# Kernel optimization log

Measured on AMD Instinct MI355X. Metric: run time of the kernel, lower is better.

The kernel has to match this reference:

```python
import jax, jax.numpy as jnp
import numpy as np
import math

B, S, H = 2, 2048, 1024
NH, DK, DV = 16, 64, 64
PAD = 0
VOCAB = 32000


def setup_inputs() -> dict:
    key = jax.random.key(0)
    ks = jax.random.split(key, 6)
    batch = jax.random.normal(ks[0], (B, S, H), dtype=jnp.float32)
    input_ids = jax.random.randint(ks[1], (B, S), 1, VOCAB)
    n_pad = S // 20
    input_ids = input_ids.at[:, S - n_pad:].set(PAD)
    init = 1.0 / math.sqrt(H)  # xavier-ish scale
    W_Q = jax.random.normal(ks[2], (H, NH * DK), dtype=jnp.float32) * init
    W_K = jax.random.normal(ks[3], (H, NH * DK), dtype=jnp.float32) * init
    W_V = jax.random.normal(ks[4], (H, NH * DV), dtype=jnp.float32) * init
    W_O = jax.random.normal(ks[5], (NH * DV, H), dtype=jnp.float32) * init
    return {
        "batch": batch, "input_ids": input_ids,
        "W_Q": W_Q, "W_K": W_K, "W_V": W_V,
        "b_Q": jnp.zeros((NH * DK,), jnp.float32),
        "b_K": jnp.zeros((NH * DK,), jnp.float32),
        "b_V": jnp.zeros((NH * DV,), jnp.float32),
        "W_O": W_O, "b_O": jnp.zeros((H,), jnp.float32),
    }


def reference(batch, input_ids, W_Q, W_K, W_V, b_Q, b_K, b_V, W_O, b_O):
    Bn, Sn, _ = batch.shape
    NEG = jnp.float32(-jnp.inf)
    # causal mask [S,S]: 0 where i>=j else -inf
    i = jnp.arange(Sn)
    causal = jnp.where(i[:, None] >= i[None, :], 0.0, NEG).astype(batch.dtype)
    # padding mask [B,1,S]: -inf at pad key positions
    pad = jnp.where(input_ids == PAD, NEG, 0.0).astype(batch.dtype)
    mask = causal[None, :, :] + pad[:, None, :]  # [B,S,S]

    Q = (batch @ W_Q + b_Q).reshape(Bn, Sn, NH, DK)
    K = (batch @ W_K + b_K).reshape(Bn, Sn, NH, DK)
    V = (batch @ W_V + b_V).reshape(Bn, Sn, NH, DV)

    scores = jnp.einsum('bqhd,bkhd->bhqk', Q, K) / math.sqrt(DK)
    attn = jax.nn.softmax(scores + mask[:, None, :, :], axis=-1)
    out = jnp.einsum('bhqk,bkhd->bqhd', attn, V).reshape(Bn, Sn, NH * DV)
    return out @ W_O + b_O
```

## Files before the change

### kernel.cpp

```cpp
#include <hip/hip_runtime.h>
#include <stdint.h>


typedef unsigned short u16;
typedef __attribute__((ext_vector_type(8))) __bf16 bf16x8;
typedef __attribute__((ext_vector_type(4))) float f32x4;
typedef __attribute__((ext_vector_type(4))) short s16x4;
typedef __attribute__((ext_vector_type(8))) short s16x8;
typedef __attribute__((ext_vector_type(2))) uint32_t u32x2;

#define SCL 0.18033688011112042f

__device__ __forceinline__ u16 f2bf(float f) {
  union { float f; uint32_t u; } v; v.f = f;
  uint32_t r = v.u + 0x7FFFu + ((v.u >> 16) & 1u);
  return (u16)(r >> 16);
}

__device__ __forceinline__ void gl_lds16(const u16* g, u16* l) {
  auto gp = reinterpret_cast<const __attribute__((address_space(1))) uint32_t*>(
      reinterpret_cast<uintptr_t>(g));
  auto lp = reinterpret_cast<__attribute__((address_space(3))) uint32_t*>(
      reinterpret_cast<uintptr_t>(l));
  __builtin_amdgcn_global_load_lds(gp, lp, 16, 0, 0);
}

__global__ void k_prologue(const float* __restrict__ batch, const int* __restrict__ ids,
                           const float* __restrict__ W_Q, const float* __restrict__ W_K,
                           const float* __restrict__ W_V, const float* __restrict__ W_O,
                           u16* __restrict__ Xbf, u16* __restrict__ dqkv, u16* __restrict__ dwo,
                           unsigned long long* __restrict__ pb) {
  __shared__ float tile[32][33];
  const int bx = blockIdx.x, t = threadIdx.x;
  if (bx < 4096) {
    int idx = (bx * 256 + t) * 4;
    const float4 v = *reinterpret_cast<const float4*>(batch + idx);
    uint2 o;
    o.x = (uint32_t)f2bf(v.x) | ((uint32_t)f2bf(v.y) << 16);
    o.y = (uint32_t)f2bf(v.z) | ((uint32_t)f2bf(v.w) << 16);
    *reinterpret_cast<uint2*>(Xbf + idx) = o;
  } else if (bx < 8192) {
    int b2 = bx - 4096;
    int z = b2 >> 10;
    b2 &= 1023;
    const float* src = z == 0 ? W_Q : (z == 1 ? W_K : (z == 2 ? W_V : W_O));
    u16* dst = z < 3 ? dqkv + (size_t)z * 1024 * 1024 : dwo;
    int c0 = (b2 & 31) * 32, r0 = (b2 >> 5) * 32;
    int tx = t & 31, ty = t >> 5;
#pragma unroll
    for (int i = 0; i < 4; ++i)
      tile[ty + i * 8][tx] = src[(size_t)(r0 + ty + i * 8) * 1024 + c0 + tx];
    __syncthreads();
#pragma unroll
    for (int i = 0; i < 4; ++i)
      dst[(size_t)(c0 + ty + i * 8) * 1024 + r0 + tx] = f2bf(tile[tx][ty + i * 8]);
  } else {
    int idx = (bx - 8192) * 4 + (t >> 6);
    int ln = t & 63;
    int b = idx >> 5, j = idx & 31;
    unsigned long long m = __ballot(ids[b * 2048 + j * 64 + ln] == 0);
    if (ln == 0) pb[idx] = m;
  }
}


__device__ __forceinline__ void gemm_tile_acc(
    const u16* __restrict__ A, const u16* __restrict__ Bt, int K,
    int tm, int tn, u16* AsA, u16* BsA, f32x4 acc[4][4]) {
  const int t = threadIdx.x, wv = t >> 6, ln = t & 63;
  const int wr = (wv & 1) * 64, wc = (wv >> 1) * 64;
  const int lr = ln & 15, q8 = (ln >> 4) * 8;
  const int srow = ln >> 2, scol = (ln & 3) * 8;

  const u16* a0 = A  + (size_t)(tm + wv * 16 + srow) * K + scol;
  const u16* a1 = A  + (size_t)(tm + (wv + 4) * 16 + srow) * K + scol;
  const u16* b0 = Bt + (size_t)(tn + wv * 16 + srow) * K + scol;
  const u16* b1 = Bt + (size_t)(tn + (wv + 4) * 16 + srow) * K + scol;
  const int l0 = wv * 512 + ln * 8, l1 = (wv + 4) * 512 + ln * 8;

#define STAGE64(k0, ho)                                   \
  {                                                       \
    gl_lds16(a0 + (k0),      AsA + (ho) + l0);            \
    gl_lds16(a1 + (k0),      AsA + (ho) + l1);            \
    gl_lds16(a0 + (k0) + 32, AsA + (ho) + 4096 + l0);     \
    gl_lds16(a1 + (k0) + 32, AsA + (ho) + 4096 + l1);     \
    gl_lds16(b0 + (k0),      BsA + (ho) + l0);            \
    gl_lds16(b1 + (k0),      BsA + (ho) + l1);            \
    gl_lds16(b0 + (k0) + 32, BsA + (ho) + 4096 + l0);     \
    gl_lds16(b1 + (k0) + 32, BsA + (ho) + 4096 + l1);     \
  }

  STAGE64(0, 0);
  __syncthreads();

  int co = 0;
  for (int k0 = 0; k0 < K; k0 += 64) {
    if (k0 + 64 < K) STAGE64(k0 + 64, co ^ 8192);
#pragma unroll
    for (int s = 0; s < 2; ++s) {
      const u16* Asb = AsA + co + s * 4096;
      const u16* Bsb = BsA + co + s * 4096;
      bf16x8 av[4], bv[4];
#pragma unroll
      for (int m = 0; m < 4; ++m)
        av[m] = *reinterpret_cast<const bf16x8*>(Asb + (wr + m * 16 + lr) * 32 + q8);
#pragma unroll
      for (int n = 0; n < 4; ++n)
        bv[n] = *reinterpret_cast<const bf16x8*>(Bsb + (wc + n * 16 + lr) * 32 + q8);
#pragma unroll
      for (int m = 0; m < 4; ++m)
#pragma unroll
        for (int n = 0; n < 4; ++n)
          acc[m][n] = __builtin_amdgcn_mfma_f32_16x16x32_bf16(av[m], bv[n], acc[m][n], 0, 0, 0);
    }
    if (k0 + 64 < K) __syncthreads();
    co ^= 8192;
  }
#undef STAGE64
}

__global__ __launch_bounds__(256) void k_qkv(
    const u16* __restrict__ X, const u16* __restrict__ Wt,
    const float* __restrict__ bQ, const float* __restrict__ bK, const float* __restrict__ bV,
    u16* __restrict__ Qt, u16* __restrict__ Kt, u16* __restrict__ Vt) {
  __shared__ __align__(16) u16 AsA[2 * 8192];
  __shared__ __align__(16) u16 BsA[2 * 8192];
  f32x4 acc[4][4] = {};
  const int tm = blockIdx.x * 128, tn = blockIdx.y * 128;
  gemm_tile_acc(X, Wt, 1024, tm, tn, AsA, BsA, acc);

  const int t = threadIdx.x, wv = t >> 6, ln = t & 63;
  const int wr = (wv & 1) * 64, wc = (wv >> 1) * 64;
  const int lr = ln & 15, q4 = (ln >> 4) * 4;
  const int which = tn >> 10;

  if (which == 0) {
#pragma unroll
    for (int n = 0; n < 4; ++n) {
      int f = (tn + wc + n * 16 + lr) & 1023;
      float bb = bQ[f];
      int h = f >> 6, dd = f & 63;
      int kh = dd >> 5, qq = (dd & 31) >> 3, e = dd & 7;
#pragma unroll
      for (int m = 0; m < 4; ++m)
#pragma unroll
        for (int r = 0; r < 4; ++r) {
          int gr = tm + wr + m * 16 + q4 + r;
          int b = gr >> 11, s = gr & 2047;
          int bh = b * 16 + h;
          size_t addr = (((size_t)(bh * 64 + (s >> 5)) * 4 + ((s & 31) >> 4) * 2 + kh) << 9) +
                        ((s & 15) + 16 * qq) * 8 + e;
          Qt[addr] = f2bf((acc[m][n][r] + bb) * SCL);
        }
    }
  } else if (which == 1) {
#pragma unroll
    for (int n = 0; n < 4; ++n) {
      int f = (tn + wc + n * 16 + lr) & 1023;
      float bb = bK[f];
      int h = f >> 6, dd = f & 63;
      int kh = dd >> 5, qq = (dd & 31) >> 3, e = dd & 7;
#pragma unroll
      for (int m = 0; m < 4; ++m)
#pragma unroll
        for (int r = 0; r < 4; ++r) {
          int gr = tm + wr + m * 16 + q4 + r;
          int b = gr >> 11, s = gr & 2047;
          int bh = b * 16 + h;
          size_t addr = (((size_t)(bh * 32 + (s >> 6)) * 8 + kh * 4 + ((s & 63) >> 4)) << 9) +
                        ((s & 15) + 16 * qq) * 8 + e;
          Kt[addr] = f2bf(acc[m][n][r] + bb);
        }
    }
  } else {
#pragma unroll
    for (int n = 0; n < 4; ++n) {
      int f = (tn + wc + n * 16 + lr) & 1023;
      float bb = bV[f];
      int h = f >> 6, dd = f & 63;
      int md = dd >> 4, iv = dd & 15;
#pragma unroll
      for (int m = 0; m < 4; ++m) {
        int gr0 = tm + wr + m * 16 + q4;
        int b = gr0 >> 11, s0 = gr0 & 2047;
        int bh = b * 16 + h;
        int j = s0 >> 6, k5 = s0 & 63;
        int mp = k5 >> 5, g = (k5 & 15) >> 2, h0 = (k5 & 16) >> 2;
        size_t addr = (((size_t)(bh * 32 + j) * 8 + mp * 4 + md) << 9) +
                      (g * 16 + iv) * 8 + h0;
        uint2 pk;
        pk.x = (uint32_t)f2bf(acc[m][n][0] + bb) | ((uint32_t)f2bf(acc[m][n][1] + bb) << 16);
        pk.y = (uint32_t)f2bf(acc[m][n][2] + bb) | ((uint32_t)f2bf(acc[m][n][3] + bb) << 16);
        *reinterpret_cast<uint2*>(Vt + addr) = pk;
      }
    }
  }
}

__global__ __launch_bounds__(256) void k_out(
    const u16* __restrict__ O, const u16* __restrict__ WoT,
    const float* __restrict__ bO, float* __restrict__ out) {
  __shared__ __align__(16) u16 AsA[2 * 8192];
  __shared__ __align__(16) u16 BsA[2 * 8192];
  f32x4 acc[4][4] = {};
  const int tm = blockIdx.x * 128, tn = blockIdx.y * 128;
  gemm_tile_acc(O, WoT, 1024, tm, tn, AsA, BsA, acc);

  const int t = threadIdx.x, wv = t >> 6, ln = t & 63;
  const int wr = (wv & 1) * 64, wc = (wv >> 1) * 64;
  const int lr = ln & 15, q4 = (ln >> 4) * 4;
#pragma unroll
  for (int n = 0; n < 4; ++n) {
    int gc = tn + wc + n * 16 + lr;
    float bb = bO[gc];
#pragma unroll
    for (int m = 0; m < 4; ++m)
#pragma unroll
      for (int r = 0; r < 4; ++r) {
        int gr = tm + wr + m * 16 + q4 + r;
        out[(size_t)gr * 1024 + gc] = acc[m][n][r] + bb;
      }
  }
}

__global__ __launch_bounds__(256, 3) void k_attn(
    const u16* __restrict__ Qt, const u16* __restrict__ Kt, const u16* __restrict__ Vt,
    const unsigned long long* __restrict__ padbits,
    u16* __restrict__ Opart, float* __restrict__ Lpart) {
  __shared__ __align__(16) u16 KsA[2 * 4096];
  __shared__ __align__(16) u16 VsA[2 * 4096];

  const int id = blockIdx.x;
  const int bh = id & 31;
  const int w = 39 - (id >> 5);
  int p, c;
  if (w < 4)       { p = w;                    c = 0; }
  else if (w < 12) { p = 4 + ((w - 4) >> 1);   c = (w - 4) & 1; }
  else if (w < 24) { p = 8 + (w - 12) / 3;     c = (w - 12) % 3; }
  else             { p = 12 + ((w - 24) >> 2); c = (w - 24) & 3; }
  const int jts = c * 8;
  const int jte = min(2 * p + 2, jts + 8);
  const int slot = bh * 40 + w;
  const int bI = bh >> 4;

  const int t = threadIdx.x, wv = t >> 6, ln = t & 63;
  const int lr = ln & 15, q4 = (ln >> 4) * 4;
  const int qbase = p * 128 + wv * 32;
  const int qrow = wv * 32;

  bf16x8 bq[2][2];
  {
    const u16* qb = Qt + (((size_t)(bh * 64 + (qbase >> 5)) * 4) << 9) + ln * 8;
#pragma unroll
    for (int n = 0; n < 2; ++n)
#pragma unroll
      for (int kh = 0; kh < 2; ++kh)
        bq[n][kh] = *reinterpret_cast<const bf16x8*>(qb + ((n * 2 + kh) << 9));
  }

  float lo[2] = {0.f, 0.f};
  f32x4 Oc[4][2] = {};

  const int st = t * 8;
  const u16* kgp = Kt + (((size_t)(bh * 32 + jts)) << 12) + st;
  const u16* vgp = Vt + (((size_t)(bh * 32 + jts)) << 12) + st;

#pragma unroll
  for (int r = 0; r < 2; ++r) {
    gl_lds16(kgp + r * 2048, &KsA[st + r * 2048]);
    gl_lds16(vgp + r * 2048, &VsA[st + r * 2048]);
  }
  __syncthreads();

  int co = 0;
  for (int j = jts; j < jte; ++j) {
    if (j + 1 < jte) {
      kgp += 4096; vgp += 4096;
      const int no = co ^ 4096;
#pragma unroll
      for (int r = 0; r < 2; ++r) {
        gl_lds16(kgp + r * 2048, &KsA[no + st + r * 2048]);
        gl_lds16(vgp + r * 2048, &VsA[no + st + r * 2048]);
      }
    }

    const int kb = j * 64;
    const unsigned long long pb = padbits[bI * 32 + j];
    const bool masked = (kb + 63 > qbase) || (pb != 0);

    f32x4 sc[4][2] = {};
#pragma unroll
    for (int m = 0; m < 4; ++m) {
      const bf16x8 ak0 = *reinterpret_cast<const bf16x8*>(&KsA[co + m * 512 + ln * 8]);
      const bf16x8 ak1 = *reinterpret_cast<const bf16x8*>(&KsA[co + (4 + m) * 512 + ln * 8]);
#pragma unroll
      for (int n = 0; n < 2; ++n) {
        sc[m][n] = __builtin_amdgcn_mfma_f32_16x16x32_bf16(ak0, bq[n][0], sc[m][n], 0, 0, 0);
        sc[m][n] = __builtin_amdgcn_mfma_f32_16x16x32_bf16(ak1, bq[n][1], sc[m][n], 0, 0, 0);
      }
    }

    s16x4 pbf[4][2];
#pragma unroll
    for (int n = 0; n < 2; ++n) {
      if (masked) {
        const int qabs = qbase + n * 16 + lr;
#pragma unroll
        for (int m = 0; m < 4; ++m)
#pragma unroll
          for (int r = 0; r < 4; ++r) {
            const int sl = m * 16 + q4 + r;
            const bool dead = (kb + sl > qabs) || ((pb >> sl) & 1ull);
            sc[m][n][r] = dead ? -1e30f : sc[m][n][r];
          }
      }
      float ps = 0.f;
#pragma unroll
      for (int m = 0; m < 4; ++m) {
        float p0 = __builtin_amdgcn_exp2f(sc[m][n][0]);
        float p1 = __builtin_amdgcn_exp2f(sc[m][n][1]);
        float p2 = __builtin_amdgcn_exp2f(sc[m][n][2]);
        float p3 = __builtin_amdgcn_exp2f(sc[m][n][3]);
        ps += (p0 + p1) + (p2 + p3);
        u32x2 pk;
        pk.x = __builtin_amdgcn_perm(__float_as_uint(p1), __float_as_uint(p0), 0x07060302);
        pk.y = __builtin_amdgcn_perm(__float_as_uint(p3), __float_as_uint(p2), 0x07060302);
        pbf[m][n] = __builtin_bit_cast(s16x4, pk);
      }
      lo[n] += ps;
    }

#pragma unroll
    for (int mp = 0; mp < 2; ++mp)
#pragma unroll
      for (int md = 0; md < 4; ++md) {
        const s16x8 vv =
            *reinterpret_cast<const s16x8*>(&VsA[co + (mp * 4 + md) * 512 + ln * 8]);
        const s16x4 vlo = __builtin_shufflevector(vv, vv, 0, 1, 2, 3);
        const s16x4 vhi = __builtin_shufflevector(vv, vv, 4, 5, 6, 7);
#pragma unroll
        for (int n = 0; n < 2; ++n) {
          Oc[md][n] = __builtin_amdgcn_mfma_f32_16x16x16bf16_1k(
              vlo, pbf[2 * mp][n], Oc[md][n], 0, 0, 0);
          Oc[md][n] = __builtin_amdgcn_mfma_f32_16x16x16bf16_1k(
              vhi, pbf[2 * mp + 1][n], Oc[md][n], 0, 0, 0);
        }
      }

    if (j + 1 < jte) __syncthreads();
    co ^= 4096;
  }

  const size_t obase = (size_t)slot * 8192;
#pragma unroll
  for (int n = 0; n < 2; ++n) {
    lo[n] += __shfl_xor(lo[n], 16, 64);
    lo[n] += __shfl_xor(lo[n], 32, 64);
    const float inv = 1.f / lo[n];
    const int qlocal = qrow + n * 16 + lr;
#pragma unroll
    for (int md = 0; md < 4; ++md) {
      uint2 pk;
      pk.x = (uint32_t)f2bf(Oc[md][n][0] * inv) | ((uint32_t)f2bf(Oc[md][n][1] * inv) << 16);
      pk.y = (uint32_t)f2bf(Oc[md][n][2] * inv) | ((uint32_t)f2bf(Oc[md][n][3] * inv) << 16);
      *reinterpret_cast<uint2*>(Opart + obase + (size_t)qlocal * 64 + md * 16 + q4) = pk;
    }
    if (ln < 16) Lpart[slot * 128 + qlocal] = lo[n];
  }
}

__global__ __launch_bounds__(256) void k_merge(
    const u16* __restrict__ Opart, const float* __restrict__ Lpart, u16* __restrict__ O) {
  const int bh = blockIdx.x >> 5, sub = blockIdx.x & 31;
  const int p = sub >> 1, half = sub & 1;
  const int nc = p < 4 ? 1 : p < 8 ? 2 : p < 12 ? 3 : 4;
  const int pre = p < 4 ? p
               : p < 8 ? 4 + (p - 4) * 2
               : p < 12 ? 12 + (p - 8) * 3
               : 24 + (p - 12) * 4;
  const int slot0 = bh * 40 + pre;

  const int t = threadIdx.x;
  const int q = half * 64 + (t >> 2), ds = (t & 3) * 16;

  float wc[4], wsum = 0.f;
  for (int cI = 0; cI < nc; ++cI) {
    wc[cI] = Lpart[(slot0 + cI) * 128 + q];
    wsum += wc[cI];
  }
  const float inv = 1.f / wsum;

  float acc[16];
#pragma unroll
  for (int e = 0; e < 16; ++e) acc[e] = 0.f;
  for (int cI = 0; cI < nc; ++cI) {
    const u16* src = Opart + (size_t)(slot0 + cI) * 8192 + q * 64 + ds;
    uint4 a = *reinterpret_cast<const uint4*>(src);
    uint4 b = *reinterpret_cast<const uint4*>(src + 8);
    uint32_t uu[8] = {a.x, a.y, a.z, a.w, b.x, b.y, b.z, b.w};
    const float wci = wc[cI];
#pragma unroll
    for (int pp = 0; pp < 8; ++pp) {
      acc[2 * pp]     += wci * __uint_as_float(uu[pp] << 16);
      acc[2 * pp + 1] += wci * __uint_as_float(uu[pp] & 0xFFFF0000u);
    }
  }

  const int bI = bh >> 4, hI = bh & 15;
  const size_t row = (size_t)(bI * 2048 + p * 128 + q);
  u16* dst = O + row * 1024 + hI * 64 + ds;
  uint32_t op[8];
#pragma unroll
  for (int pp = 0; pp < 8; ++pp)
    op[pp] = (uint32_t)f2bf(acc[2 * pp] * inv) | ((uint32_t)f2bf(acc[2 * pp + 1] * inv) << 16);
  *reinterpret_cast<uint4*>(dst) = *reinterpret_cast<const uint4*>(&op[0]);
  *reinterpret_cast<uint4*>(dst + 8) = *reinterpret_cast<const uint4*>(&op[4]);
}


extern "C" void kernel_launch(void* const* d_in, const int* in_sizes, int n_in,
                              void* d_out, int out_size, void* d_ws, size_t ws_size,
                              hipStream_t stream) {
  (void)in_sizes; (void)n_in; (void)out_size; (void)ws_size;
  const float* batch = (const float*)d_in[0];
  const int* ids     = (const int*)d_in[1];
  const float* W_Q   = (const float*)d_in[2];
  const float* W_K   = (const float*)d_in[3];
  const float* W_V   = (const float*)d_in[4];
  const float* b_Q   = (const float*)d_in[5];
  const float* b_K   = (const float*)d_in[6];
  const float* b_V   = (const float*)d_in[7];
  const float* W_O   = (const float*)d_in[8];
  const float* b_O   = (const float*)d_in[9];
  float* out = (float*)d_out;

  u16* ws = (u16*)d_ws;
  u16* Xbf   = ws;
  u16* WqkvT = Xbf + 4194304;
  u16* WoT   = WqkvT + 3145728;
  u16* Qtb   = WoT + 1048576;
  u16* Ktb   = Qtb + 4194304;
  u16* Vtb   = Ktb + 4194304;
  u16* Opart = Vtb + 4194304;
  float* Lpart = (float*)WqkvT;
  u16* Ob    = Xbf;

  unsigned long long* padbits =
      (unsigned long long*)((char*)d_out + (size_t)out_size * 4 - 512);

  k_prologue<<<8208, 256, 0, stream>>>(batch, ids, W_Q, W_K, W_V, W_O, Xbf, WqkvT, WoT, padbits);
  k_qkv<<<dim3(32, 24), 256, 0, stream>>>(Xbf, WqkvT, b_Q, b_K, b_V, Qtb, Ktb, Vtb);
  k_attn<<<1280, 256, 0, stream>>>(Qtb, Ktb, Vtb, padbits, Opart, Lpart);
  k_merge<<<1024, 256, 0, stream>>>(Opart, Lpart, Ob);
  k_out<<<dim3(32, 8), 256, 0, stream>>>(Ob, WoT, b_O, out);
}
```

Measured before the change: 177.4 us.

## Fuse split-KV partial merge into output projection GEMM A-tile staging

Removes the separate k_merge kernel and has k_out read partial attention outputs and their softmax denominators directly. The A operand for each K-slice is built on the fly as a weighted combination of the partial outputs, converted to bf16 and written into LDS, while the W_O slice is still loaded asynchronously into LDS. This drops one kernel launch and the round trip of the merged O tensor through global memory. In exchange, each of the 8 column blocks recomputes the merge for its row tile, and the A staging becomes synchronous register work that may not overlap with the MFMA loop as well as async loads do.

After: 223.8 us. 26.2% more time.

```diff
diff --git a/kernel.cpp b/kernel.cpp
--- a/kernel.cpp
+++ b/kernel.cpp
@@ -198,20 +198,123 @@
 }
 
 __global__ __launch_bounds__(256) void k_out(
-    const u16* __restrict__ O, const u16* __restrict__ WoT,
-    const float* __restrict__ bO, float* __restrict__ out) {
+    const u16* __restrict__ Opart, const float* __restrict__ Lpart,
+    const u16* __restrict__ WoT, const float* __restrict__ bO, float* __restrict__ out) {
   __shared__ __align__(16) u16 AsA[2 * 8192];
   __shared__ __align__(16) u16 BsA[2 * 8192];
   f32x4 acc[4][4] = {};
   const int tm = blockIdx.x * 128, tn = blockIdx.y * 128;
-  gemm_tile_acc(O, WoT, 1024, tm, tn, AsA, BsA, acc);
 
   const int t = threadIdx.x, wv = t >> 6, ln = t & 63;
-  const int wr = (wv & 1) * 64, wc = (wv >> 1) * 64;
-  const int lr = ln & 15, q4 = (ln >> 4) * 4;
+  const int wr = (wv & 1) * 64, wcn = (wv >> 1) * 64;
+  const int lr = ln & 15, q8 = (ln >> 4) * 8, q4 = (ln >> 4) * 4;
+  const int srow = ln >> 2, scol = (ln & 3) * 8;
+
+  const int b = tm >> 11, p = (tm & 2047) >> 7;
+  const int nc = p < 4 ? 1 : p < 8 ? 2 : p < 12 ? 3 : 4;
+  const int pre = p < 4 ? p
+               : p < 8 ? 4 + (p - 4) * 2
+               : p < 12 ? 12 + (p - 8) * 3
+               : 24 + (p - 12) * 4;
+  const int q0 = wv * 16 + srow, q1 = (wv + 4) * 16 + srow;
+  const int l0 = wv * 512 + ln * 8, l1 = (wv + 4) * 512 + ln * 8;
+
+  const u16* b0 = WoT + (size_t)(tn + wv * 16 + srow) * 1024 + scol;
+  const u16* b1 = WoT + (size_t)(tn + (wv + 4) * 16 + srow) * 1024 + scol;
+
+  auto stageA = [&](int k0, int ho) {
+    const int h = k0 >> 6;
+    const int slotb = (b * 16 + h) * 40 + pre;
+    const float* lp = Lpart + (size_t)slotb * 128;
+    float w0[4], w1[4];
+    float s0 = 0.f, s1 = 0.f;
+#pragma unroll
+    for (int c = 0; c < 4; ++c)
+      if (c < nc) {
+        w0[c] = lp[c * 128 + q0]; s0 += w0[c];
+        w1[c] = lp[c * 128 + q1]; s1 += w1[c];
+      }
+    const float inv0 = 1.f / s0, inv1 = 1.f / s1;
+    const u16* ob = Opart + (size_t)slotb * 8192;
+#pragma unroll
+    for (int s = 0; s < 2; ++s) {
+      const int d0 = s * 32 + scol;
+      float a0v[8], a1v[8];
+#pragma unroll
+      for (int e = 0; e < 8; ++e) { a0v[e] = 0.f; a1v[e] = 0.f; }
+#pragma unroll
+      for (int c = 0; c < 4; ++c)
+        if (c < nc) {
+          const uint4 x0 = *reinterpret_cast<const uint4*>(ob + c * 8192 + q0 * 64 + d0);
+          const uint4 x1 = *reinterpret_cast<const uint4*>(ob + c * 8192 + q1 * 64 + d0);
+          const uint32_t u0[4] = {x0.x, x0.y, x0.z, x0.w};
+          const uint32_t u1[4] = {x1.x, x1.y, x1.z, x1.w};
+#pragma unroll
+          for (int pp = 0; pp < 4; ++pp) {
+            a0v[2 * pp]     += w0[c] * __uint_as_float(u0[pp] << 16);
+            a0v[2 * pp + 1] += w0[c] * __uint_as_float(u0[pp] & 0xFFFF0000u);
+            a1v[2 * pp]     += w1[c] * __uint_as_float(u1[pp] << 16);
+            a1v[2 * pp + 1] += w1[c] * __uint_as_float(u1[pp] & 0xFFFF0000u);
+          }
+        }
+      uint32_t o0[4], o1[4];
+#pragma unroll
+      for (int pp = 0; pp < 4; ++pp) {
+        o0[pp] = (uint32_t)f2bf(a0v[2 * pp] * inv0) |
+                 ((uint32_t)f2bf(a0v[2 * pp + 1] * inv0) << 16);
+        o1[pp] = (uint32_t)f2bf(a1v[2 * pp] * inv1) |
+                 ((uint32_t)f2bf(a1v[2 * pp + 1] * inv1) << 16);
+      }
+      *reinterpret_cast<uint4*>(&AsA[ho + s * 4096 + l0]) =
+          *reinterpret_cast<const uint4*>(o0);
+      *reinterpret_cast<uint4*>(&AsA[ho + s * 4096 + l1]) =
+          *reinterpret_cast<const uint4*>(o1);
+    }
+  };
+
+#define STAGE64B(k0, ho)                                  \
+  {                                                       \
+    gl_lds16(b0 + (k0),      BsA + (ho) + l0);            \
+    gl_lds16(b1 + (k0),      BsA + (ho) + l1);            \
+    gl_lds16(b0 + (k0) + 32, BsA + (ho) + 4096 + l0);     \
+    gl_lds16(b1 + (k0) + 32, BsA + (ho) + 4096 + l1);     \
+  }
+
+  STAGE64B(0, 0);
+  stageA(0, 0);
+  __syncthreads();
+
+  int co = 0;
+  for (int k0 = 0; k0 < 1024; k0 += 64) {
+    if (k0 + 64 < 1024) {
+      STAGE64B(k0 + 64, co ^ 8192);
+      stageA(k0 + 64, co ^ 8192);
+    }
+#pragma unroll
+    for (int s = 0; s < 2; ++s) {
+      const u16* Asb = AsA + co + s * 4096;
+      const u16* Bsb = BsA + co + s * 4096;
+      bf16x8 av[4], bv[4];
+#pragma unroll
+      for (int m = 0; m < 4; ++m)
+        av[m] = *reinterpret_cast<const bf16x8*>(Asb + (wr + m * 16 + lr) * 32 + q8);
+#pragma unroll
+      for (int n = 0; n < 4; ++n)
+        bv[n] = *reinterpret_cast<const bf16x8*>(Bsb + (wcn + n * 16 + lr) * 32 + q8);
+#pragma unroll
+      for (int m = 0; m < 4; ++m)
+#pragma unroll
+        for (int n = 0; n < 4; ++n)
+          acc[m][n] = __builtin_amdgcn_mfma_f32_16x16x32_bf16(av[m], bv[n], acc[m][n], 0, 0, 0);
+    }
+    if (k0 + 64 < 1024) __syncthreads();
+    co ^= 8192;
+  }
+#undef STAGE64B
+
 #pragma unroll
   for (int n = 0; n < 4; ++n) {
-    int gc = tn + wc + n * 16 + lr;
+    int gc = tn + wcn + n * 16 + lr;
     float bb = bO[gc];
 #pragma unroll
     for (int m = 0; m < 4; ++m)
@@ -367,54 +470,6 @@
     }
     if (ln < 16) Lpart[slot * 128 + qlocal] = lo[n];
   }
-}
-
-__global__ __launch_bounds__(256) void k_merge(
-    const u16* __restrict__ Opart, const float* __restrict__ Lpart, u16* __restrict__ O) {
-  const int bh = blockIdx.x >> 5, sub = blockIdx.x & 31;
-  const int p = sub >> 1, half = sub & 1;
-  const int nc = p < 4 ? 1 : p < 8 ? 2 : p < 12 ? 3 : 4;
-  const int pre = p < 4 ? p
-               : p < 8 ? 4 + (p - 4) * 2
-               : p < 12 ? 12 + (p - 8) * 3
-               : 24 + (p - 12) * 4;
-  const int slot0 = bh * 40 + pre;
-
-  const int t = threadIdx.x;
-  const int q = half * 64 + (t >> 2), ds = (t & 3) * 16;
-
-  float wc[4], wsum = 0.f;
-  for (int cI = 0; cI < nc; ++cI) {
-    wc[cI] = Lpart[(slot0 + cI) * 128 + q];
-    wsum += wc[cI];
-  }
-  const float inv = 1.f / wsum;
-
-  float acc[16];
-#pragma unroll
-  for (int e = 0; e < 16; ++e) acc[e] = 0.f;
-  for (int cI = 0; cI < nc; ++cI) {
-    const u16* src = Opart + (size_t)(slot0 + cI) * 8192 + q * 64 + ds;
-    uint4 a = *reinterpret_cast<const uint4*>(src);
-    uint4 b = *reinterpret_cast<const uint4*>(src + 8);
-    uint32_t uu[8] = {a.x, a.y, a.z, a.w, b.x, b.y, b.z, b.w};
-    const float wci = wc[cI];
-#pragma unroll
-    for (int pp = 0; pp < 8; ++pp) {
-      acc[2 * pp]     += wci * __uint_as_float(uu[pp] << 16);
-      acc[2 * pp + 1] += wci * __uint_as_float(uu[pp] & 0xFFFF0000u);
-    }
-  }
-
-  const int bI = bh >> 4, hI = bh & 15;
-  const size_t row = (size_t)(bI * 2048 + p * 128 + q);
-  u16* dst = O + row * 1024 + hI * 64 + ds;
-  uint32_t op[8];
-#pragma unroll
-  for (int pp = 0; pp < 8; ++pp)
-    op[pp] = (uint32_t)f2bf(acc[2 * pp] * inv) | ((uint32_t)f2bf(acc[2 * pp + 1] * inv) << 16);
-  *reinterpret_cast<uint4*>(dst) = *reinterpret_cast<const uint4*>(&op[0]);
-  *reinterpret_cast<uint4*>(dst + 8) = *reinterpret_cast<const uint4*>(&op[4]);
 }
 
 
@@ -443,7 +498,6 @@
   u16* Vtb   = Ktb + 4194304;
   u16* Opart = Vtb + 4194304;
   float* Lpart = (float*)WqkvT;
-  u16* Ob    = Xbf;
 
   unsigned long long* padbits =
       (unsigned long long*)((char*)d_out + (size_t)out_size * 4 - 512);
@@ -451,6 +505,5 @@
   k_prologue<<<8208, 256, 0, stream>>>(batch, ids, W_Q, W_K, W_V, W_O, Xbf, WqkvT, WoT, padbits);
   k_qkv<<<dim3(32, 24), 256, 0, stream>>>(Xbf, WqkvT, b_Q, b_K, b_V, Qtb, Ktb, Vtb);
   k_attn<<<1280, 256, 0, stream>>>(Qtb, Ktb, Vtb, padbits, Opart, Lpart);
-  k_merge<<<1024, 256, 0, stream>>>(Opart, Lpart, Ob);
-  k_out<<<dim3(32, 8), 256, 0, stream>>>(Ob, WoT, b_O, out);
-}
+  k_out<<<dim3(32, 8), 256, 0, stream>>>(Opart, Lpart, WoT, b_O, out);
+}
```
